# Kernel optimization log

Hardware: AMD Instinct MI355X
Metric: run time of the kernel (lower is better)

The kernel has to match this reference:

```python
import jax, jax.numpy as jnp
import numpy as np

B, NIN, NOUT, E = 4, 50000, 50000, 819200
CIN, COUT, H = 16, 16, 100


def _lin(key, fan_in, fan_out):
    k1, k2 = jax.random.split(key)
    s = 1.0 / np.sqrt(fan_in)
    w = jax.random.uniform(k1, (fan_in, fan_out), jnp.float32, -s, s)
    b = jax.random.uniform(k2, (fan_out,), jnp.float32, -s, s)
    return w, b


def setup_inputs() -> dict:
    key = jax.random.key(0)
    ks = jax.random.split(key, 12)
    inp = {}
    inp["x"] = jax.random.normal(ks[0], (B, NIN * CIN), jnp.float32)
    inp["inp_positions"] = jax.random.uniform(ks[1], (NIN, 3), jnp.float32)
    inp["out_positions"] = jax.random.uniform(ks[2], (NOUT, 3), jnp.float32)
    inp["edge_src"] = jax.random.randint(ks[3], (E,), 0, NIN)
    inp["edge_dst"] = jax.random.randint(ks[4], (E,), 0, NOUT)
    # edge-MLP: Linear(6,100) -> ReLU -> Linear(100,100) -> ReLU -> Linear(100,100) -> ReLU -> Linear(100, CIN*COUT)
    inp["w1"], inp["b1"] = _lin(ks[5], 6, H)
    inp["w2"], inp["b2"] = _lin(ks[6], H, H)
    inp["w3"], inp["b3"] = _lin(ks[7], H, H)
    inp["w4"], inp["b4"] = _lin(ks[8], H, CIN * COUT)
    inp["root"], _ = _lin(ks[9], CIN, COUT)  # NNConv root weight
    inp["bias"] = jax.random.uniform(ks[10], (COUT,), jnp.float32, -0.05, 0.05)
    return inp


def reference(x, inp_positions, out_positions, w1, b1, w2, b2, w3, b3, w4, b4, root, bias, edge_src, edge_dst):
    # x: (B, NIN*CIN) -> node features of input nodes; output nodes get zero features
    xb = x.reshape(B, NIN, CIN)
    # edge attributes: cat(out_pos[dst], in_pos[src]) -> (E, 6)
    e_attr = jnp.concatenate([out_positions[edge_dst], inp_positions[edge_src]], axis=1)
    # per-edge MLP producing edge-conditioned weight matrix (E, CIN, COUT)
    h = jax.nn.relu(e_attr @ w1 + b1)
    h = jax.nn.relu(h @ w2 + b2)
    h = jax.nn.relu(h @ w3 + b3)
    W = (h @ w4 + b4).reshape(E, CIN, COUT)
    # gather source features, apply edge-specific matmul -> messages (E, B, COUT)
    x_src = xb[:, edge_src]  # (B, E, CIN)
    msg = jnp.einsum('bei,eio->ebo', x_src, W)
    # mean-aggregate into destination (output) nodes
    agg = jax.ops.segment_sum(msg.reshape(E, B * COUT), edge_dst, num_segments=NOUT)
    deg = jax.ops.segment_sum(jnp.ones((E,), jnp.float32), edge_dst, num_segments=NOUT)
    agg = (agg / jnp.clip(deg, 1.0)[:, None]).reshape(NOUT, B, COUT)
    # root-weight term: destination node features are zeros -> contributes zero; bias remains
    out = jnp.transpose(agg, (1, 0, 2)) + bias  # (B, NOUT, COUT)
    return out
```

## Files before the change

### kernel.cpp

```cpp
#include <hip/hip_runtime.h>
#include <hip/hip_bf16.h>
#include <cstdint>

constexpr int B_    = 4;
constexpr int NIN_  = 50000;
constexpr int NOUT_ = 50000;
constexpr int E_    = 819200;
constexpr int CI    = 16;
constexpr int CO    = 16;
constexpr int Hh    = 100;

constexpr int M      = 32;
constexpr int NBLK   = 256;
constexpr int NTILES = E_ / M;
constexpr int BITER  = NTILES / 8;
constexpr size_t LDS_BYTES = 163840;

typedef __attribute__((ext_vector_type(8))) short bf16x8;
typedef __attribute__((ext_vector_type(4))) float f32x4;

union frag { bf16x8 v; unsigned u[4]; };

__device__ inline unsigned pk2(float a, float b) {
    unsigned r;
    asm("v_cvt_pk_bf16_f32 %0, %1, %2" : "=v"(r) : "v"(a), "v"(b));
    return r;
}

__device__ inline int chunkXor(int r) { return ((r & 7) << 3) ^ ((r & 8) << 1); }
__device__ inline int swz(int r, int k) { return r * 128 + (k ^ chunkXor(r)); }


__global__ __launch_bounds__(256)
void prep_kernel(const float* __restrict__ w1, const float* __restrict__ w2,
                 const float* __restrict__ w3, const float* __restrict__ w4,
                 const float* __restrict__ b1, const float* __restrict__ b2,
                 const float* __restrict__ b3, const float* __restrict__ b4,
                 unsigned short* __restrict__ wcat, unsigned short* __restrict__ W1T,
                 float* __restrict__ b1p, float* __restrict__ b2p,
                 float* __restrict__ b3p, float* __restrict__ b4p)
{
    const int i = blockIdx.x * 256 + threadIdx.x;
    auto bf = [](float f) {
        __hip_bfloat16 h = __float2bfloat16(f);
        return *reinterpret_cast<unsigned short*>(&h);
    };
    auto inv = [](int kpos) {
        return ((kpos >> 2) & 1) * 64 + ((kpos >> 5) & 3) * 16 +
               ((kpos >> 3) & 3) * 4 + (kpos & 3);
    };
    if (i < 32768) {
        int j = i & 16383; int r = j >> 7, kz = j & 127;
        int kpos = kz ^ chunkXor(r);
        int u = inv(kpos);
        const float* w = (i < 16384) ? w2 : w3;
        wcat[i] = (r < Hh && u < Hh) ? bf(w[u * Hh + r]) : (unsigned short)0;
    } else if (i < 65536) {
        int j = i - 32768; int r = j >> 7, kz = j & 127;
        int kpos = kz ^ chunkXor(r);
        int u = inv(kpos);
        wcat[i] = (u < Hh) ? bf(w4[u * 256 + r]) : (unsigned short)0;
    } else if (i < 69632) {
        int j = i - 65536; int wi = j >> 5, k = j & 31;
        W1T[j] = (k < 6 && wi < Hh) ? bf(w1[k * Hh + wi]) : (unsigned short)0;
    } else if (i < 69760) { int j = i - 69632; b1p[j] = (j < Hh) ? b1[j] : 0.f; }
    else if (i < 69888) { int j = i - 69760; b2p[j] = (j < Hh) ? b2[j] : 0.f; }
    else if (i < 70016) { int j = i - 69888; b3p[j] = (j < Hh) ? b3[j] : 0.f; }
    else if (i < 70272) { int j = i - 70016; b4p[j] = b4[j]; }
}

__device__ inline void hidden_layer(const unsigned short* __restrict__ Wl,
                                    const float* __restrict__ bp,
                                    const frag (&in)[2][4], frag (&out)[2][4],
                                    int cl, int kg)
{
    #pragma unroll
    for (int nt = 0; nt < 8; ++nt) {
        bf16x8 wf[4];
        #pragma unroll
        for (int ks = 0; ks < 4; ++ks)
            wf[ks] = *reinterpret_cast<const bf16x8*>(
                Wl + swz(nt * 16 + cl, ks * 32 + kg * 8));
        f32x4 bias = *reinterpret_cast<const f32x4*>(bp + nt * 16 + kg * 4);
        #pragma unroll
        for (int et = 0; et < 2; ++et) {
            f32x4 acc = bias;
            #pragma unroll
            for (int ks = 0; ks < 4; ++ks)
                acc = __builtin_amdgcn_mfma_f32_16x16x32_bf16(wf[ks], in[et][ks].v, acc, 0, 0, 0);
            out[et][nt & 3].u[((nt >> 2) << 1) + 0] = pk2(fmaxf(acc[0], 0.f), fmaxf(acc[1], 0.f));
            out[et][nt & 3].u[((nt >> 2) << 1) + 1] = pk2(fmaxf(acc[2], 0.f), fmaxf(acc[3], 0.f));
        }
    }
}

__global__ __launch_bounds__(512, 2)
void edge_kernel(const float* __restrict__ x, const float* __restrict__ ipos,
                 const float* __restrict__ opos, const int* __restrict__ esrc,
                 const int* __restrict__ edst,
                 const unsigned short* __restrict__ wcat,
                 const unsigned short* __restrict__ W1T,
                 const float* __restrict__ b1p, const float* __restrict__ b2p,
                 const float* __restrict__ b3p, const float* __restrict__ b4p,
                 float* __restrict__ agg, float* __restrict__ deg)
{
    extern __shared__ char lds[];
    unsigned short* Wlds = (unsigned short*)lds;

    const int tid  = threadIdx.x;
    const int wv   = __builtin_amdgcn_readfirstlane(tid >> 6);
    const int lane = tid & 63;
    const int cl   = lane & 15;
    const int kg   = lane >> 4;

    int srcv, dstv; unsigned au0, au1, au2;
    {
        const int e0 = (blockIdx.x * 8 + wv) * M;
        const int eA = e0 + (lane & 31);
        srcv = esrc[eA]; dstv = edst[eA];
        if (lane < 32) atomicAdd(&deg[dstv], 1.0f);
        float o0 = opos[dstv * 3 + 0], o1 = opos[dstv * 3 + 1], o2 = opos[dstv * 3 + 2];
        float i0 = ipos[srcv * 3 + 0], i1 = ipos[srcv * 3 + 1], i2 = ipos[srcv * 3 + 2];
        au0 = pk2(o0, o1); au1 = pk2(o2, i0); au2 = pk2(i1, i2);
    }

    {
        const float4* s4 = (const float4*)wcat;
        float4* d4 = (float4*)lds;
        for (int i = tid; i < 8192; i += 512) d4[i] = s4[i];
    }
    bf16x8 a1w[8];
    #pragma unroll
    for (int nt = 0; nt < 8; ++nt)
        a1w[nt] = *reinterpret_cast<const bf16x8*>(W1T + (nt * 16 + cl) * 32 + kg * 8);
    __syncthreads();

    uint2* xs = (uint2*)(lds + 131072 + wv * 4096);

    for (int bt = blockIdx.x; bt < BITER; bt += NBLK) {
        float4 xg[4][2];
        {
            const int ih = lane >> 5;
            const float* xp0 = x + (size_t)srcv * CI + ih * 8;
            #pragma unroll
            for (int b = 0; b < 4; ++b) {
                const float* xp = xp0 + (size_t)b * (NIN_ * CI);
                xg[b][0] = *reinterpret_cast<const float4*>(xp);
                xg[b][1] = *reinterpret_cast<const float4*>(xp + 4);
            }
        }

        frag b1f[2];
        #pragma unroll
        for (int et = 0; et < 2; ++et) {
            const int sl = et * 16 + cl;
            unsigned s0 = __shfl(au0, sl), s1 = __shfl(au1, sl), s2 = __shfl(au2, sl);
            frag f;
            f.u[0] = (kg == 0) ? s0 : 0u;
            f.u[1] = (kg == 0) ? s1 : 0u;
            f.u[2] = (kg == 0) ? s2 : 0u;
            f.u[3] = 0u;
            b1f[et] = f;
        }

        frag B2[2][4];
        #pragma unroll
        for (int nt = 0; nt < 8; ++nt) {
            f32x4 bias = *reinterpret_cast<const f32x4*>(b1p + nt * 16 + kg * 4);
            #pragma unroll
            for (int et = 0; et < 2; ++et) {
                f32x4 acc = bias;
                acc = __builtin_amdgcn_mfma_f32_16x16x32_bf16(a1w[nt], b1f[et].v, acc, 0, 0, 0);
                B2[et][nt & 3].u[((nt >> 2) << 1) + 0] = pk2(fmaxf(acc[0], 0.f), fmaxf(acc[1], 0.f));
                B2[et][nt & 3].u[((nt >> 2) << 1) + 1] = pk2(fmaxf(acc[2], 0.f), fmaxf(acc[3], 0.f));
            }
        }

        int nsrc = srcv, ndst = dstv;
        unsigned na0 = au0, na1 = au1, na2 = au2;
        {
            const int nbt = bt + NBLK;
            if (nbt < BITER) {
                const int ne0 = (nbt * 8 + wv) * M;
                const int neA = ne0 + (lane & 31);
                nsrc = esrc[neA]; ndst = edst[neA];
                if (lane < 32) atomicAdd(&deg[ndst], 1.0f);
                float o0 = opos[ndst * 3 + 0], o1 = opos[ndst * 3 + 1], o2 = opos[ndst * 3 + 2];
                float i0 = ipos[nsrc * 3 + 0], i1 = ipos[nsrc * 3 + 1], i2 = ipos[nsrc * 3 + 2];
                na0 = pk2(o0, o1); na1 = pk2(o2, i0); na2 = pk2(i1, i2);
            }
        }

        frag B3[2][4];
        hidden_layer(Wlds, b2p, B2, B3, cl, kg);

        {
            const int ih = lane >> 5;
            const int e  = lane & 31;
            #pragma unroll
            for (int i2 = 0; i2 < 2; ++i2)
                #pragma unroll
                for (int r = 0; r < 4; ++r) {
                    uint2 v;
                    v.x = pk2(xg[0][i2][r], xg[1][i2][r]);
                    v.y = pk2(xg[2][i2][r], xg[3][i2][r]);
                    xs[(ih * 8 + i2 * 4 + r) * 32 + e] = v;
                }
        }

        frag B4[2][4];
        hidden_layer(Wlds + 16384, b3p, B3, B4, cl, kg);

        float macc[2][16];
        #pragma unroll
        for (int et = 0; et < 2; ++et)
            #pragma unroll
            for (int q = 0; q < 16; ++q) macc[et][q] = 0.f;

        const unsigned short* W4l = Wlds + 32768;
        #pragma unroll
        for (int nt = 0; nt < 16; ++nt) {
            bf16x8 wf[4];
            #pragma unroll
            for (int ks = 0; ks < 4; ++ks)
                wf[ks] = *reinterpret_cast<const bf16x8*>(
                    W4l + swz(nt * 16 + cl, ks * 32 + kg * 8));
            const float bv = b4p[nt * 16 + cl];
            #pragma unroll
            for (int et = 0; et < 2; ++et) {
                const uint4 xa = *reinterpret_cast<const uint4*>(
                    &xs[nt * 32 + et * 16 + kg * 4]);
                const uint4 xb = *reinterpret_cast<const uint4*>(
                    &xs[nt * 32 + et * 16 + kg * 4 + 2]);
                f32x4 acc = {bv, bv, bv, bv};
                #pragma unroll
                for (int ks = 0; ks < 4; ++ks)
                    acc = __builtin_amdgcn_mfma_f32_16x16x32_bf16(B4[et][ks].v, wf[ks], acc, 0, 0, 0);
                const unsigned w01[4] = {xa.x, xa.z, xb.x, xb.z};
                const unsigned w23[4] = {xa.y, xa.w, xb.y, xb.w};
                #pragma unroll
                for (int j = 0; j < 4; ++j) {
                    const float x0 = __uint_as_float(w01[j] << 16);
                    const float x1 = __uint_as_float(w01[j] & 0xffff0000u);
                    const float x2 = __uint_as_float(w23[j] << 16);
                    const float x3 = __uint_as_float(w23[j] & 0xffff0000u);
                    macc[et][0 * 4 + j] = fmaf(x0, acc[j], macc[et][0 * 4 + j]);
                    macc[et][1 * 4 + j] = fmaf(x1, acc[j], macc[et][1 * 4 + j]);
                    macc[et][2 * 4 + j] = fmaf(x2, acc[j], macc[et][2 * 4 + j]);
                    macc[et][3 * 4 + j] = fmaf(x3, acc[j], macc[et][3 * 4 + j]);
                }
            }
        }

        #pragma unroll
        for (int et = 0; et < 2; ++et)
            #pragma unroll
            for (int j = 0; j < 4; ++j) {
                const int d = __shfl(dstv, et * 16 + kg * 4 + j);
                float* p = agg + (size_t)d * (B_ * CO) + cl;
                #pragma unroll
                for (int b = 0; b < 4; ++b)
                    atomicAdd(p + b * 16, macc[et][b * 4 + j]);
            }

        srcv = nsrc; dstv = ndst; au0 = na0; au1 = na1; au2 = na2;
    }
}

__global__ __launch_bounds__(256)
void finalize_kernel(const float* __restrict__ agg, const float* __restrict__ deg,
                     const float* __restrict__ bias, float* __restrict__ out)
{
    const int idx = blockIdx.x * 256 + threadIdx.x;
    if (idx >= B_ * NOUT_ * CO) return;
    const int o = idx & 15;
    const int n = (idx >> 4) % NOUT_;
    const int b = idx / (NOUT_ * CO);
    const float d = fmaxf(deg[n], 1.0f);
    out[idx] = agg[(size_t)n * (B_ * CO) + b * CO + o] / d + bias[o];
}

extern "C" void kernel_launch(void* const* d_in, const int* in_sizes, int n_in,
                              void* d_out, int out_size, void* d_ws, size_t ws_size,
                              hipStream_t stream)
{
    const float* x    = (const float*)d_in[0];
    const float* ipos = (const float*)d_in[1];
    const float* opos = (const float*)d_in[2];
    const int*   esrc = (const int*)d_in[3];
    const int*   edst = (const int*)d_in[4];
    const float* w1   = (const float*)d_in[5];
    const float* b1   = (const float*)d_in[6];
    const float* w2   = (const float*)d_in[7];
    const float* b2   = (const float*)d_in[8];
    const float* w3   = (const float*)d_in[9];
    const float* b3   = (const float*)d_in[10];
    const float* w4   = (const float*)d_in[11];
    const float* b4   = (const float*)d_in[12];
    const float* bias = (const float*)d_in[14];

    char* ob = (char*)d_out;
    unsigned short* wcat = (unsigned short*)ob;
    unsigned short* W1T  = (unsigned short*)(ob + 131072);
    float* b1p = (float*)(ob + 139264);
    float* b2p = (float*)(ob + 139776);
    float* b3p = (float*)(ob + 140288);
    float* b4p = (float*)(ob + 140800);

    float* agg = (float*)d_ws;
    float* deg = agg + (size_t)NOUT_ * (B_ * CO);

    hipMemsetAsync(d_ws, 0,
                   ((size_t)NOUT_ * (B_ * CO) + NOUT_) * sizeof(float), stream);

    prep_kernel<<<275, 256, 0, stream>>>(w1, w2, w3, w4, b1, b2, b3, b4,
                                         wcat, W1T, b1p, b2p, b3p, b4p);

    hipFuncSetAttribute(reinterpret_cast<const void*>(edge_kernel),
                        hipFuncAttributeMaxDynamicSharedMemorySize,
                        (int)LDS_BYTES);
    edge_kernel<<<NBLK, 512, LDS_BYTES, stream>>>(
        x, ipos, opos, esrc, edst, wcat, W1T, b1p, b2p, b3p, b4p, agg, deg);

    const int total = B_ * NOUT_ * CO;
    finalize_kernel<<<(total + 255) / 256, 256, 0, stream>>>(agg, deg, bias,
                                                             (float*)d_out);
}
```

Measured before the change: 359.7 us.

## Process 64 edges per wave, split x staging in halves, re-layout agg

Each wave now handles 64 edges (four 16-edge tiles) instead of 32, so every LDS weight fragment is reused across twice as many MFMAs. The x gather is split into two halves staged through LDS separately to fit the larger tile, and the layer-1 weights are reloaded per iteration instead of kept in registers. The agg buffer is re-laid out as (B, NOUT, CO) so finalize becomes a vectorized float4 pass using a reciprocal multiply. Register pressure rises considerably (macc and the B2/B3/B4 fragment arrays double), which risks spills or lower occupancy.

```diff
diff --git a/kernel.cpp b/kernel.cpp
--- a/kernel.cpp
+++ b/kernel.cpp
@@ -10,10 +10,8 @@
 constexpr int CO    = 16;
 constexpr int Hh    = 100;
 
-constexpr int M      = 32;
 constexpr int NBLK   = 256;
-constexpr int NTILES = E_ / M;
-constexpr int BITER  = NTILES / 8;
+constexpr int BITER  = E_ / 512;
 constexpr size_t LDS_BYTES = 163840;
 
 typedef __attribute__((ext_vector_type(8))) short bf16x8;
@@ -69,10 +67,10 @@
     else if (i < 70272) { int j = i - 70016; b4p[j] = b4[j]; }
 }
 
-__device__ inline void hidden_layer(const unsigned short* __restrict__ Wl,
-                                    const float* __restrict__ bp,
-                                    const frag (&in)[2][4], frag (&out)[2][4],
-                                    int cl, int kg)
+__device__ inline void hidden_layer4(const unsigned short* __restrict__ Wl,
+                                     const float* __restrict__ bp,
+                                     const frag (&in)[4][4], frag (&out)[4][4],
+                                     int cl, int kg)
 {
     #pragma unroll
     for (int nt = 0; nt < 8; ++nt) {
@@ -83,7 +81,7 @@
                 Wl + swz(nt * 16 + cl, ks * 32 + kg * 8));
         f32x4 bias = *reinterpret_cast<const f32x4*>(bp + nt * 16 + kg * 4);
         #pragma unroll
-        for (int et = 0; et < 2; ++et) {
+        for (int et = 0; et < 4; ++et) {
             f32x4 acc = bias;
             #pragma unroll
             for (int ks = 0; ks < 4; ++ks)
@@ -115,10 +113,9 @@
 
     int srcv, dstv; unsigned au0, au1, au2;
     {
-        const int e0 = (blockIdx.x * 8 + wv) * M;
-        const int eA = e0 + (lane & 31);
+        const int eA = (blockIdx.x * 8 + wv) * 64 + lane;
         srcv = esrc[eA]; dstv = edst[eA];
-        if (lane < 32) atomicAdd(&deg[dstv], 1.0f);
+        atomicAdd(&deg[dstv], 1.0f);
         float o0 = opos[dstv * 3 + 0], o1 = opos[dstv * 3 + 1], o2 = opos[dstv * 3 + 2];
         float i0 = ipos[srcv * 3 + 0], i1 = ipos[srcv * 3 + 1], i2 = ipos[srcv * 3 + 2];
         au0 = pk2(o0, o1); au1 = pk2(o2, i0); au2 = pk2(i1, i2);
@@ -129,30 +126,30 @@
         float4* d4 = (float4*)lds;
         for (int i = tid; i < 8192; i += 512) d4[i] = s4[i];
     }
-    bf16x8 a1w[8];
-    #pragma unroll
-    for (int nt = 0; nt < 8; ++nt)
-        a1w[nt] = *reinterpret_cast<const bf16x8*>(W1T + (nt * 16 + cl) * 32 + kg * 8);
     __syncthreads();
 
     uint2* xs = (uint2*)(lds + 131072 + wv * 4096);
 
     for (int bt = blockIdx.x; bt < BITER; bt += NBLK) {
-        float4 xg[4][2];
+        float4 xg0[4][2];
         {
-            const int ih = lane >> 5;
-            const float* xp0 = x + (size_t)srcv * CI + ih * 8;
+            const float* xp = x + (size_t)srcv * CI;
             #pragma unroll
             for (int b = 0; b < 4; ++b) {
-                const float* xp = xp0 + (size_t)b * (NIN_ * CI);
-                xg[b][0] = *reinterpret_cast<const float4*>(xp);
-                xg[b][1] = *reinterpret_cast<const float4*>(xp + 4);
-            }
-        }
-
-        frag b1f[2];
-        #pragma unroll
-        for (int et = 0; et < 2; ++et) {
+                const float* xb = xp + (size_t)b * (NIN_ * CI);
+                xg0[b][0] = *reinterpret_cast<const float4*>(xb);
+                xg0[b][1] = *reinterpret_cast<const float4*>(xb + 4);
+            }
+        }
+        bf16x8 a1w[8];
+        #pragma unroll
+        for (int nt = 0; nt < 8; ++nt)
+            a1w[nt] = *reinterpret_cast<const bf16x8*>(
+                W1T + (nt * 16 + cl) * 32 + kg * 8);
+
+        frag b1f[4];
+        #pragma unroll
+        for (int et = 0; et < 4; ++et) {
             const int sl = et * 16 + cl;
             unsigned s0 = __shfl(au0, sl), s1 = __shfl(au1, sl), s2 = __shfl(au2, sl);
             frag f;
@@ -163,12 +160,12 @@
             b1f[et] = f;
         }
 
-        frag B2[2][4];
+        frag B2[4][4];
         #pragma unroll
         for (int nt = 0; nt < 8; ++nt) {
             f32x4 bias = *reinterpret_cast<const f32x4*>(b1p + nt * 16 + kg * 4);
             #pragma unroll
-            for (int et = 0; et < 2; ++et) {
+            for (int et = 0; et < 4; ++et) {
                 f32x4 acc = bias;
                 acc = __builtin_amdgcn_mfma_f32_16x16x32_bf16(a1w[nt], b1f[et].v, acc, 0, 0, 0);
                 B2[et][nt & 3].u[((nt >> 2) << 1) + 0] = pk2(fmaxf(acc[0], 0.f), fmaxf(acc[1], 0.f));
@@ -181,45 +178,51 @@
         {
             const int nbt = bt + NBLK;
             if (nbt < BITER) {
-                const int ne0 = (nbt * 8 + wv) * M;
-                const int neA = ne0 + (lane & 31);
+                const int neA = (nbt * 8 + wv) * 64 + lane;
                 nsrc = esrc[neA]; ndst = edst[neA];
-                if (lane < 32) atomicAdd(&deg[ndst], 1.0f);
+                atomicAdd(&deg[ndst], 1.0f);
                 float o0 = opos[ndst * 3 + 0], o1 = opos[ndst * 3 + 1], o2 = opos[ndst * 3 + 2];
                 float i0 = ipos[nsrc * 3 + 0], i1 = ipos[nsrc * 3 + 1], i2 = ipos[nsrc * 3 + 2];
                 na0 = pk2(o0, o1); na1 = pk2(o2, i0); na2 = pk2(i1, i2);
             }
         }
 
-        frag B3[2][4];
-        hidden_layer(Wlds, b2p, B2, B3, cl, kg);
-
+        frag B3[4][4];
+        hidden_layer4(Wlds, b2p, B2, B3, cl, kg);
+
+        float4 xg1[4][2];
         {
-            const int ih = lane >> 5;
-            const int e  = lane & 31;
-            #pragma unroll
-            for (int i2 = 0; i2 < 2; ++i2)
-                #pragma unroll
-                for (int r = 0; r < 4; ++r) {
-                    uint2 v;
-                    v.x = pk2(xg[0][i2][r], xg[1][i2][r]);
-                    v.y = pk2(xg[2][i2][r], xg[3][i2][r]);
-                    xs[(ih * 8 + i2 * 4 + r) * 32 + e] = v;
-                }
-        }
-
-        frag B4[2][4];
-        hidden_layer(Wlds + 16384, b3p, B3, B4, cl, kg);
-
-        float macc[2][16];
-        #pragma unroll
-        for (int et = 0; et < 2; ++et)
+            const float* xp = x + (size_t)srcv * CI + 8;
+            #pragma unroll
+            for (int b = 0; b < 4; ++b) {
+                const float* xb = xp + (size_t)b * (NIN_ * CI);
+                xg1[b][0] = *reinterpret_cast<const float4*>(xb);
+                xg1[b][1] = *reinterpret_cast<const float4*>(xb + 4);
+            }
+        }
+
+        frag B4[4][4];
+        hidden_layer4(Wlds + 16384, b3p, B3, B4, cl, kg);
+
+        float macc[4][16];
+        #pragma unroll
+        for (int et = 0; et < 4; ++et)
             #pragma unroll
             for (int q = 0; q < 16; ++q) macc[et][q] = 0.f;
 
         const unsigned short* W4l = Wlds + 32768;
-        #pragma unroll
-        for (int nt = 0; nt < 16; ++nt) {
+
+        #pragma unroll
+        for (int i2 = 0; i2 < 2; ++i2)
+            #pragma unroll
+            for (int r = 0; r < 4; ++r) {
+                uint2 v;
+                v.x = pk2(xg0[0][i2][r], xg0[1][i2][r]);
+                v.y = pk2(xg0[2][i2][r], xg0[3][i2][r]);
+                xs[(i2 * 4 + r) * 64 + lane] = v;
+            }
+        #pragma unroll
+        for (int nt = 0; nt < 8; ++nt) {
             bf16x8 wf[4];
             #pragma unroll
             for (int ks = 0; ks < 4; ++ks)
@@ -227,23 +230,25 @@
                     W4l + swz(nt * 16 + cl, ks * 32 + kg * 8));
             const float bv = b4p[nt * 16 + cl];
             #pragma unroll
-            for (int et = 0; et < 2; ++et) {
+            for (int et = 0; et < 4; ++et) {
                 const uint4 xa = *reinterpret_cast<const uint4*>(
-                    &xs[nt * 32 + et * 16 + kg * 4]);
-                const uint4 xb = *reinterpret_cast<const uint4*>(
-                    &xs[nt * 32 + et * 16 + kg * 4 + 2]);
+                    &xs[nt * 64 + et * 16 + kg * 4]);
                 f32x4 acc = {bv, bv, bv, bv};
                 #pragma unroll
                 for (int ks = 0; ks < 4; ++ks)
                     acc = __builtin_amdgcn_mfma_f32_16x16x32_bf16(B4[et][ks].v, wf[ks], acc, 0, 0, 0);
-                const unsigned w01[4] = {xa.x, xa.z, xb.x, xb.z};
-                const unsigned w23[4] = {xa.y, xa.w, xb.y, xb.w};
+                const unsigned w01[4] = {xa.x, xa.z, 0, 0};
+                const uint4 xb = *reinterpret_cast<const uint4*>(
+                    &xs[nt * 64 + et * 16 + kg * 4 + 2]);
+                const unsigned w01b[4] = {xa.x, xa.z, xb.x, xb.z};
+                const unsigned w23b[4] = {xa.y, xa.w, xb.y, xb.w};
+                (void)w01;
                 #pragma unroll
                 for (int j = 0; j < 4; ++j) {
-                    const float x0 = __uint_as_float(w01[j] << 16);
-                    const float x1 = __uint_as_float(w01[j] & 0xffff0000u);
-                    const float x2 = __uint_as_float(w23[j] << 16);
-                    const float x3 = __uint_as_float(w23[j] & 0xffff0000u);
+                    const float x0 = __uint_as_float(w01b[j] << 16);
+                    const float x1 = __uint_as_float(w01b[j] & 0xffff0000u);
+                    const float x2 = __uint_as_float(w23b[j] << 16);
+                    const float x3 = __uint_as_float(w23b[j] & 0xffff0000u);
                     macc[et][0 * 4 + j] = fmaf(x0, acc[j], macc[et][0 * 4 + j]);
                     macc[et][1 * 4 + j] = fmaf(x1, acc[j], macc[et][1 * 4 + j]);
                     macc[et][2 * 4 + j] = fmaf(x2, acc[j], macc[et][2 * 4 + j]);
@@ -253,14 +258,58 @@
         }
 
         #pragma unroll
-        for (int et = 0; et < 2; ++et)
+        for (int i2 = 0; i2 < 2; ++i2)
+            #pragma unroll
+            for (int r = 0; r < 4; ++r) {
+                uint2 v;
+                v.x = pk2(xg1[0][i2][r], xg1[1][i2][r]);
+                v.y = pk2(xg1[2][i2][r], xg1[3][i2][r]);
+                xs[(i2 * 4 + r) * 64 + lane] = v;
+            }
+        #pragma unroll
+        for (int nt8 = 0; nt8 < 8; ++nt8) {
+            const int nt = 8 + nt8;
+            bf16x8 wf[4];
+            #pragma unroll
+            for (int ks = 0; ks < 4; ++ks)
+                wf[ks] = *reinterpret_cast<const bf16x8*>(
+                    W4l + swz(nt * 16 + cl, ks * 32 + kg * 8));
+            const float bv = b4p[nt * 16 + cl];
+            #pragma unroll
+            for (int et = 0; et < 4; ++et) {
+                const uint4 xa = *reinterpret_cast<const uint4*>(
+                    &xs[nt8 * 64 + et * 16 + kg * 4]);
+                const uint4 xb = *reinterpret_cast<const uint4*>(
+                    &xs[nt8 * 64 + et * 16 + kg * 4 + 2]);
+                f32x4 acc = {bv, bv, bv, bv};
+                #pragma unroll
+                for (int ks = 0; ks < 4; ++ks)
+                    acc = __builtin_amdgcn_mfma_f32_16x16x32_bf16(B4[et][ks].v, wf[ks], acc, 0, 0, 0);
+                const unsigned w01b[4] = {xa.x, xa.z, xb.x, xb.z};
+                const unsigned w23b[4] = {xa.y, xa.w, xb.y, xb.w};
+                #pragma unroll
+                for (int j = 0; j < 4; ++j) {
+                    const float x0 = __uint_as_float(w01b[j] << 16);
+                    const float x1 = __uint_as_float(w01b[j] & 0xffff0000u);
+                    const float x2 = __uint_as_float(w23b[j] << 16);
+                    const float x3 = __uint_as_float(w23b[j] & 0xffff0000u);
+                    macc[et][0 * 4 + j] = fmaf(x0, acc[j], macc[et][0 * 4 + j]);
+                    macc[et][1 * 4 + j] = fmaf(x1, acc[j], macc[et][1 * 4 + j]);
+                    macc[et][2 * 4 + j] = fmaf(x2, acc[j], macc[et][2 * 4 + j]);
+                    macc[et][3 * 4 + j] = fmaf(x3, acc[j], macc[et][3 * 4 + j]);
+                }
+            }
+        }
+
+        #pragma unroll
+        for (int et = 0; et < 4; ++et)
             #pragma unroll
             for (int j = 0; j < 4; ++j) {
                 const int d = __shfl(dstv, et * 16 + kg * 4 + j);
-                float* p = agg + (size_t)d * (B_ * CO) + cl;
                 #pragma unroll
                 for (int b = 0; b < 4; ++b)
-                    atomicAdd(p + b * 16, macc[et][b * 4 + j]);
+                    atomicAdd(agg + (size_t)b * (NOUT_ * CO) + (size_t)d * CO + cl,
+                              macc[et][b * 4 + j]);
             }
 
         srcv = nsrc; dstv = ndst; au0 = na0; au1 = na1; au2 = na2;
@@ -271,13 +320,17 @@
 void finalize_kernel(const float* __restrict__ agg, const float* __restrict__ deg,
                      const float* __restrict__ bias, float* __restrict__ out)
 {
-    const int idx = blockIdx.x * 256 + threadIdx.x;
-    if (idx >= B_ * NOUT_ * CO) return;
-    const int o = idx & 15;
-    const int n = (idx >> 4) % NOUT_;
-    const int b = idx / (NOUT_ * CO);
-    const float d = fmaxf(deg[n], 1.0f);
-    out[idx] = agg[(size_t)n * (B_ * CO) + b * CO + o] / d + bias[o];
+    const int idx4 = blockIdx.x * 256 + threadIdx.x;
+    const int n = (idx4 >> 2) % NOUT_;
+    const float4 a = reinterpret_cast<const float4*>(agg)[idx4];
+    const float dinv = 1.0f / fmaxf(deg[n], 1.0f);
+    const float4 bv = reinterpret_cast<const float4*>(bias)[idx4 & 3];
+    float4 o;
+    o.x = a.x * dinv + bv.x;
+    o.y = a.y * dinv + bv.y;
+    o.z = a.z * dinv + bv.z;
+    o.w = a.w * dinv + bv.w;
+    reinterpret_cast<float4*>(out)[idx4] = o;
 }
 
 extern "C" void kernel_launch(void* const* d_in, const int* in_sizes, int n_in,
@@ -308,10 +361,10 @@
     float* b4p = (float*)(ob + 140800);
 
     float* agg = (float*)d_ws;
-    float* deg = agg + (size_t)NOUT_ * (B_ * CO);
+    float* deg = agg + (size_t)B_ * NOUT_ * CO;
 
     hipMemsetAsync(d_ws, 0,
-                   ((size_t)NOUT_ * (B_ * CO) + NOUT_) * sizeof(float), stream);
+                   ((size_t)B_ * NOUT_ * CO + NOUT_) * sizeof(float), stream);
 
     prep_kernel<<<275, 256, 0, stream>>>(w1, w2, w3, w4, b1, b2, b3, b4,
                                          wcat, W1T, b1p, b2p, b3p, b4p);
@@ -322,7 +375,6 @@
     edge_kernel<<<NBLK, 512, LDS_BYTES, stream>>>(
         x, ipos, opos, esrc, edst, wcat, W1T, b1p, b2p, b3p, b4p, agg, deg);
 
-    const int total = B_ * NOUT_ * CO;
-    finalize_kernel<<<(total + 255) / 256, 256, 0, stream>>>(agg, deg, bias,
-                                                             (float*)d_out);
-}
+    finalize_kernel<<<B_ * NOUT_ * CO / 4 / 256, 256, 0, stream>>>(
+        agg, deg, bias, (float*)d_out);
+}
```

After: 397.4 us. 1.1x slower.
